# Kernel tuning notes

Measured on AMD Instinct MI355X. Metric: run time of the kernel, lower is better.

## Reference

```python
import jax, jax.numpy as jnp
import numpy as np

EPS = 1e-5

def _layernorm(x, gamma, beta):
    mu = jnp.mean(x, axis=-1, keepdims=True)
    var = jnp.var(x, axis=-1, keepdims=True)
    return (x - mu) * jax.lax.rsqrt(var + EPS) * gamma + beta

def setup_inputs() -> dict:
    key = jax.random.key(0)
    ks = jax.random.split(key, 6)
    bs, t, dim = 4, 2048, 1024
    x = jax.random.normal(ks[0], (bs, t, dim), dtype=jnp.float32)
    # shared LayerNorm params (same module applied twice in forward)
    ln_gamma = jnp.ones((dim,), dtype=jnp.float32)
    ln_beta = jnp.zeros((dim,), dtype=jnp.float32)
    # Linear params, stored as (in, out)
    w1 = jax.random.normal(ks[1], (dim, 2 * dim), dtype=jnp.float32) / np.sqrt(dim)
    b1 = jax.random.normal(ks[2], (2 * dim,), dtype=jnp.float32) * 0.01
    w2 = jax.random.normal(ks[3], (2 * dim, dim), dtype=jnp.float32) / np.sqrt(2 * dim)
    b2 = jax.random.normal(ks[4], (dim,), dtype=jnp.float32) * 0.01
    return {"x": x, "ln_gamma": ln_gamma, "ln_beta": ln_beta,
            "w1": w1, "b1": b1, "w2": w2, "b2": b2}

def reference(x, ln_gamma, ln_beta, w1, b1, w2, b2):
    # x: [bs, t, f]
    y = _layernorm(x, ln_gamma, ln_beta)
    y = jax.nn.gelu(jnp.einsum('btf,fh->bth', y, w1) + b1, approximate=False)
    y = jnp.einsum('bth,hf->btf', y, w2) + b2
    # attention-like quadratic mix (no softmax): (x @ x^T) @ y
    scores = jnp.einsum('btf,bsf->bts', x, x)          # [bs, t, t]
    y = jnp.einsum('bts,bsf->btf', scores, y)
    y = x + y
    y = _layernorm(y, ln_gamma, ln_beta)
    return y
```

## Files before the change

kernel.cpp:

```cpp
#include <hip/hip_runtime.h>
#include <hip/hip_fp16.h>

typedef _Float16 f16;
typedef _Float16 f16x8 __attribute__((ext_vector_type(8)));
typedef _Float16 f16x4 __attribute__((ext_vector_type(4)));
typedef float f32x4 __attribute__((ext_vector_type(4)));

#define LN_EPS 1e-5f

__device__ __forceinline__ float erf_fast(float x) {
    const float ax = __builtin_fabsf(x);
    const float t = 1.0f / (1.0f + 0.3275911f * ax);
    const float y = t * (0.254829592f +
                    t * (-0.284496736f +
                    t * (1.421413741f +
                    t * (-1.453152027f +
                    t * 1.061405429f))));
    const float r = 1.0f - y * __expf(-ax * ax);
    return __builtin_copysignf(r, x);
}

__device__ __forceinline__ float gelu_exact(float v) {
    return 0.5f * v * (1.0f + erf_fast(v * 0.70710678118654752440f));
}

__device__ __forceinline__ void gload_lds16(const f16* g, f16* l) {
    __builtin_amdgcn_global_load_lds(
        (const __attribute__((address_space(1))) unsigned int*)(g),
        (__attribute__((address_space(3))) unsigned int*)(l),
        16, 0, 0);
}

__global__ __launch_bounds__(256)
void ln_cast_kernel(const float* __restrict__ x,
                    const float* __restrict__ gamma,
                    const float* __restrict__ beta,
                    f16* __restrict__ y_h,
                    f16* __restrict__ x_h) {
    const int row = blockIdx.x;
    const int t = threadIdx.x;
    const size_t base = (size_t)row * 1024;
    float4 v = ((const float4*)(x + base))[t];
    float s  = v.x + v.y + v.z + v.w;
    float s2 = v.x*v.x + v.y*v.y + v.z*v.z + v.w*v.w;
    #pragma unroll
    for (int off = 32; off > 0; off >>= 1) {
        s  += __shfl_down(s, off, 64);
        s2 += __shfl_down(s2, off, 64);
    }
    __shared__ float ls[4], ls2[4];
    const int wid = t >> 6;
    if ((t & 63) == 0) { ls[wid] = s; ls2[wid] = s2; }
    __syncthreads();
    if (t == 0) {
        ls[0]  = ls[0] + ls[1] + ls[2] + ls[3];
        ls2[0] = ls2[0] + ls2[1] + ls2[2] + ls2[3];
    }
    __syncthreads();
    const float mu   = ls[0] * (1.0f / 1024.0f);
    const float var  = ls2[0] * (1.0f / 1024.0f) - mu * mu;
    const float rstd = rsqrtf(var + LN_EPS);
    const float4 g  = ((const float4*)gamma)[t];
    const float4 bt = ((const float4*)beta)[t];
    f16x4 yo, xo;
    yo[0] = (f16)((v.x - mu) * rstd * g.x + bt.x);
    yo[1] = (f16)((v.y - mu) * rstd * g.y + bt.y);
    yo[2] = (f16)((v.z - mu) * rstd * g.z + bt.z);
    yo[3] = (f16)((v.w - mu) * rstd * g.w + bt.w);
    xo[0] = (f16)v.x; xo[1] = (f16)v.y; xo[2] = (f16)v.z; xo[3] = (f16)v.w;
    *(f16x4*)(y_h + base + t * 4) = yo;
    *(f16x4*)(x_h + base + t * 4) = xo;
}

__global__ __launch_bounds__(256)
void ln_final_kernel(const float* __restrict__ pre,
                     const float* __restrict__ gamma,
                     const float* __restrict__ beta,
                     float* __restrict__ out) {
    const int row = blockIdx.x;
    const int t = threadIdx.x;
    const size_t base = (size_t)row * 1024;
    float4 v = ((const float4*)(pre + base))[t];
    float s  = v.x + v.y + v.z + v.w;
    float s2 = v.x*v.x + v.y*v.y + v.z*v.z + v.w*v.w;
    #pragma unroll
    for (int off = 32; off > 0; off >>= 1) {
        s  += __shfl_down(s, off, 64);
        s2 += __shfl_down(s2, off, 64);
    }
    __shared__ float ls[4], ls2[4];
    const int wid = t >> 6;
    if ((t & 63) == 0) { ls[wid] = s; ls2[wid] = s2; }
    __syncthreads();
    if (t == 0) {
        ls[0]  = ls[0] + ls[1] + ls[2] + ls[3];
        ls2[0] = ls2[0] + ls2[1] + ls2[2] + ls2[3];
    }
    __syncthreads();
    const float mu   = ls[0] * (1.0f / 1024.0f);
    const float var  = ls2[0] * (1.0f / 1024.0f) - mu * mu;
    const float rstd = rsqrtf(var + LN_EPS);
    const float4 g  = ((const float4*)gamma)[t];
    const float4 bt = ((const float4*)beta)[t];
    float4 o;
    o.x = (v.x - mu) * rstd * g.x + bt.x;
    o.y = (v.y - mu) * rstd * g.y + bt.y;
    o.z = (v.z - mu) * rstd * g.z + bt.z;
    o.w = (v.w - mu) * rstd * g.w + bt.w;
    ((float4*)(out + base))[t] = o;
}

__global__ __launch_bounds__(256)
void transpose_cast_kernel(const float* __restrict__ src,
                           f16* __restrict__ dst, int R, int C) {
    __shared__ float tile[32][33];
    const int c0 = blockIdx.x * 32, r0 = blockIdx.y * 32;
    const int tx = threadIdx.x & 31, ty = threadIdx.x >> 5;
    #pragma unroll
    for (int i = 0; i < 4; ++i) {
        const int r = ty + i * 8;
        tile[r][tx] = src[(size_t)(r0 + r) * C + c0 + tx];
    }
    __syncthreads();
    #pragma unroll
    for (int i = 0; i < 4; ++i) {
        const int r = ty + i * 8;
        dst[(size_t)(c0 + r) * R + r0 + tx] = (f16)tile[tx][r];
    }
}

__global__ __launch_bounds__(256)
void transpose_f16_kernel(const f16* __restrict__ src,
                          f16* __restrict__ dst, int R, int C) {
    __shared__ f16 tile[32][33];
    const size_t zb = (size_t)blockIdx.z * R * C;
    src += zb; dst += zb;
    const int c0 = blockIdx.x * 32, r0 = blockIdx.y * 32;
    const int tx = threadIdx.x & 31, ty = threadIdx.x >> 5;
    #pragma unroll
    for (int i = 0; i < 4; ++i) {
        const int r = ty + i * 8;
        tile[r][tx] = src[(size_t)(r0 + r) * C + c0 + tx];
    }
    __syncthreads();
    #pragma unroll
    for (int i = 0; i < 4; ++i) {
        const int r = ty + i * 8;
        dst[(size_t)(c0 + r) * R + r0 + tx] = tile[tx][r];
    }
}

template <int EPI>
__global__ __launch_bounds__(512, 2)
void gemm256x128_nt_kernel(const f16* __restrict__ A, const f16* __restrict__ Bt,
                           const float* __restrict__ bias,
                           const float* __restrict__ xadd,
                           f16* __restrict__ outH, float* __restrict__ outF,
                           int M, int N, int K,
                           long long batchA, long long batchB, long long batchC) {
    __shared__ __attribute__((aligned(16))) f16 sA[3][256 * 64];
    __shared__ __attribute__((aligned(16))) f16 sB[3][128 * 64];

    const int z = blockIdx.z;
    A  += (size_t)z * batchA;
    Bt += (size_t)z * batchB;

    const int m0 = blockIdx.x * 256;
    const int n0 = blockIdx.y * 128;
    const int t = threadIdx.x;
    const int l = t & 63;
    const int wid = t >> 6;
    const int wr = wid >> 1;
    const int wc = wid & 1;
    const int rl = l & 15;
    const int g  = l >> 4;
    const int nk = K >> 6;

    const int rowS = t >> 3;
    const int kbS  = ((t & 7) ^ (rowS & 7)) * 8;
    const f16* pA = A  + (size_t)(m0 + rowS) * K + kbS;
    const f16* pB = Bt + (size_t)(n0 + rowS) * K + kbS;
    const int ldsS = wid * 512;

    const int rA = wr * 64 + rl;
    const int rB = wc * 64 + rl;
    const int swk0 = ((g)     ^ (rl & 7)) * 8;
    const int swk1 = ((4 + g) ^ (rl & 7)) * 8;

    f32x4 acc[4][4] = {};

    auto mf = [&](f32x4 c, f16x8 af, f16x8 bf) {
        if constexpr (EPI != 1)
            return __builtin_amdgcn_mfma_f32_16x16x32_f16(bf, af, c, 0, 0, 0);
        else
            return __builtin_amdgcn_mfma_f32_16x16x32_f16(af, bf, c, 0, 0, 0);
    };

    auto stgA = [&](f16* dst, int u, int kc) {
        gload_lds16(pA + (size_t)u * 64 * K + kc * 64, dst + u * 4096 + ldsS);
    };
    auto stgB = [&](f16* dst, int u, int kc) {
        gload_lds16(pB + (size_t)u * 64 * K + kc * 64, dst + u * 4096 + ldsS);
    };

    const int t1 = (nk > 1) ? 1 : 0;
    #pragma unroll
    for (int u = 0; u < 4; ++u) stgA(sA[0], u, 0);
    #pragma unroll
    for (int u = 0; u < 2; ++u) stgB(sB[0], u, 0);
    #pragma unroll
    for (int u = 0; u < 4; ++u) stgA(sA[1], u, t1);
    #pragma unroll
    for (int u = 0; u < 2; ++u) stgB(sB[1], u, t1);

    f16 *curA = sA[0], *nxtA = sA[1], *farA = sA[2];
    f16 *curB = sB[0], *nxtB = sB[1], *farB = sB[2];

    f16x8 a[4][2], b[4][2];

    for (int kt = 0; kt < nk; ++kt) {
        asm volatile("s_waitcnt vmcnt(6)" ::: "memory");
        __builtin_amdgcn_s_barrier();

        const int kt2 = (kt + 2 < nk) ? kt + 2 : nk - 1;

        #pragma unroll
        for (int fm = 0; fm < 2; ++fm) {
            a[fm][0] = *(const f16x8*)(curA + (rA + fm * 16) * 64 + swk0);
            a[fm][1] = *(const f16x8*)(curA + (rA + fm * 16) * 64 + swk1);
        }
        #pragma unroll
        for (int fn = 0; fn < 2; ++fn) {
            b[fn][0] = *(const f16x8*)(curB + (rB + fn * 16) * 64 + swk0);
            b[fn][1] = *(const f16x8*)(curB + (rB + fn * 16) * 64 + swk1);
        }
        stgA(farA, 0, kt2);
        stgA(farA, 1, kt2);
        asm volatile("s_waitcnt lgkmcnt(0)" ::: "memory");
        __builtin_amdgcn_sched_barrier(0);
        __builtin_amdgcn_s_setprio(1);
        #pragma unroll
        for (int fm = 0; fm < 2; ++fm)
            #pragma unroll
            for (int fn = 0; fn < 2; ++fn) {
                acc[fm][fn] = mf(acc[fm][fn], a[fm][0], b[fn][0]);
                acc[fm][fn] = mf(acc[fm][fn], a[fm][1], b[fn][1]);
            }
        __builtin_amdgcn_s_setprio(0);

        #pragma unroll
        for (int fn = 2; fn < 4; ++fn) {
            b[fn][0] = *(const f16x8*)(curB + (rB + fn * 16) * 64 + swk0);
            b[fn][1] = *(const f16x8*)(curB + (rB + fn * 16) * 64 + swk1);
        }
        stgA(farA, 2, kt2);
        stgA(farA, 3, kt2);
        asm volatile("s_waitcnt lgkmcnt(0)" ::: "memory");
        __builtin_amdgcn_sched_barrier(0);
        __builtin_amdgcn_s_setprio(1);
        #pragma unroll
        for (int fm = 0; fm < 2; ++fm)
            #pragma unroll
            for (int fn = 2; fn < 4; ++fn) {
                acc[fm][fn] = mf(acc[fm][fn], a[fm][0], b[fn][0]);
                acc[fm][fn] = mf(acc[fm][fn], a[fm][1], b[fn][1]);
            }
        __builtin_amdgcn_s_setprio(0);

        #pragma unroll
        for (int fm = 2; fm < 4; ++fm) {
            a[fm][0] = *(const f16x8*)(curA + (rA + fm * 16) * 64 + swk0);
            a[fm][1] = *(const f16x8*)(curA + (rA + fm * 16) * 64 + swk1);
        }
        stgB(farB, 0, kt2);
        stgB(farB, 1, kt2);
        asm volatile("s_waitcnt lgkmcnt(0)" ::: "memory");
        __builtin_amdgcn_sched_barrier(0);
        __builtin_amdgcn_s_setprio(1);
        #pragma unroll
        for (int fm = 2; fm < 4; ++fm)
            #pragma unroll
            for (int fn = 2; fn < 4; ++fn) {
                acc[fm][fn] = mf(acc[fm][fn], a[fm][0], b[fn][0]);
                acc[fm][fn] = mf(acc[fm][fn], a[fm][1], b[fn][1]);
            }
        __builtin_amdgcn_s_setprio(0);

        __builtin_amdgcn_s_setprio(1);
        #pragma unroll
        for (int fm = 2; fm < 4; ++fm)
            #pragma unroll
            for (int fn = 0; fn < 2; ++fn) {
                acc[fm][fn] = mf(acc[fm][fn], a[fm][0], b[fn][0]);
                acc[fm][fn] = mf(acc[fm][fn], a[fm][1], b[fn][1]);
            }
        __builtin_amdgcn_s_setprio(0);

        f16* tp;
        tp = curA; curA = nxtA; nxtA = farA; farA = tp;
        tp = curB; curB = nxtB; nxtB = farB; farB = tp;
    }
    asm volatile("s_waitcnt vmcnt(0)" ::: "memory");

    if (EPI == 1) {
        #pragma unroll
        for (int fm = 0; fm < 4; ++fm) {
            #pragma unroll
            for (int fn = 0; fn < 4; ++fn) {
                const int col = n0 + wc * 64 + fn * 16 + rl;
                const int row0 = m0 + wr * 64 + fm * 16 + g * 4;
                const int zz = row0 >> 11;
                const int rr = row0 & 2047;
                const float bv = bias[col];
                f16x4 o;
                #pragma unroll
                for (int r = 0; r < 4; ++r) o[r] = (f16)(acc[fm][fn][r] + bv);
                *(f16x4*)(outH + ((size_t)zz * N + col) * 2048 + rr) = o;
            }
        }
    } else {
        const float* xaddz = xadd;
        float* outFz = outF;
        if (EPI == 3) {
            outFz += (size_t)z * batchC;
            xaddz += (size_t)z * batchC;
        }
        #pragma unroll
        for (int fm = 0; fm < 4; ++fm) {
            const int row = m0 + wr * 64 + fm * 16 + rl;
            #pragma unroll
            for (int fn = 0; fn < 4; ++fn) {
                const int colb = n0 + wc * 64 + fn * 16 + g * 4;
                if (EPI == 0) {
                    const float4 bv = *(const float4*)&bias[colb];
                    f16x4 o;
                    o[0] = (f16)gelu_exact(acc[fm][fn][0] + bv.x);
                    o[1] = (f16)gelu_exact(acc[fm][fn][1] + bv.y);
                    o[2] = (f16)gelu_exact(acc[fm][fn][2] + bv.z);
                    o[3] = (f16)gelu_exact(acc[fm][fn][3] + bv.w);
                    *(f16x4*)(outH + (size_t)row * N + colb) = o;
                } else {
                    const size_t idx = (size_t)row * N + colb;
                    const float4 xa = *(const float4*)&xaddz[idx];
                    float4 o;
                    o.x = acc[fm][fn][0] + xa.x;
                    o.y = acc[fm][fn][1] + xa.y;
                    o.z = acc[fm][fn][2] + xa.z;
                    o.w = acc[fm][fn][3] + xa.w;
                    *(float4*)(outFz + idx) = o;
                }
            }
        }
    }
}

__global__ __launch_bounds__(256, 3)
void gemm_nt_kernel(const f16* __restrict__ A, const f16* __restrict__ Bt,
                    f16* __restrict__ outH,
                    int M, int N, int K,
                    long long batchA, long long batchB, long long batchC) {
    __shared__ __attribute__((aligned(16))) f16 sA[3][128 * 32];
    __shared__ __attribute__((aligned(16))) f16 sB[3][128 * 32];

    const int z = blockIdx.z;
    A  += (size_t)z * batchA;
    Bt += (size_t)z * batchB;

    const int m0 = blockIdx.x * 128;
    const int n0 = blockIdx.y * 128;
    const int t = threadIdx.x;
    const int l = t & 63;
    const int wid = t >> 6;
    const int wm = (wid >> 1) * 64;
    const int wn = (wid & 1) * 64;

    f32x4 acc[4][4] = {};

    const int rl = l & 15;
    const int nk = K >> 5;

    const int row0 = t >> 2;
    const int kb = ((t & 3) ^ (row0 & 3)) * 8;
    const f16* Ag0 = A  + (size_t)(m0 + row0) * K + kb;
    const f16* Ag1 = A  + (size_t)(m0 + row0 + 64) * K + kb;
    const f16* Bg0 = Bt + (size_t)(n0 + row0) * K + kb;
    const f16* Bg1 = Bt + (size_t)(n0 + row0 + 64) * K + kb;
    const int lo0 = wid * 512;
    const int lo1 = 2048 + wid * 512;

    const int swk = (((l >> 4) ^ (rl & 3))) * 8;

    gload_lds16(Ag0,      sA[0] + lo0);
    gload_lds16(Ag1,      sA[0] + lo1);
    gload_lds16(Bg0,      sB[0] + lo0);
    gload_lds16(Bg1,      sB[0] + lo1);
    gload_lds16(Ag0 + 32, sA[1] + lo0);
    gload_lds16(Ag1 + 32, sA[1] + lo1);
    gload_lds16(Bg0 + 32, sB[1] + lo0);
    gload_lds16(Bg1 + 32, sB[1] + lo1);

    f16 *curA = sA[0], *nxtA = sA[1], *farA = sA[2];
    f16 *curB = sB[0], *nxtB = sB[1], *farB = sB[2];

    for (int kt = 0; kt < nk; ++kt) {
        asm volatile("s_waitcnt vmcnt(4)" ::: "memory");
        __builtin_amdgcn_s_barrier();

        const int ktn = (kt + 2 < nk) ? kt + 2 : nk - 1;
        const int kof = ktn * 32;
        gload_lds16(Ag0 + kof, farA + lo0);
        gload_lds16(Ag1 + kof, farA + lo1);
        gload_lds16(Bg0 + kof, farB + lo0);
        gload_lds16(Bg1 + kof, farB + lo1);

        f16x8 a[4], b[4];
        #pragma unroll
        for (int f = 0; f < 4; ++f) {
            a[f] = *(const f16x8*)&curA[(wm + f * 16 + rl) * 32 + swk];
            b[f] = *(const f16x8*)&curB[(wn + f * 16 + rl) * 32 + swk];
        }
        #pragma unroll
        for (int fm = 0; fm < 4; ++fm)
            #pragma unroll
            for (int fn = 0; fn < 4; ++fn)
                acc[fm][fn] = __builtin_amdgcn_mfma_f32_16x16x32_f16(
                    b[fn], a[fm], acc[fm][fn], 0, 0, 0);

        f16* tA = curA; curA = nxtA; nxtA = farA; farA = tA;
        f16* tB = curB; curB = nxtB; nxtB = farB; farB = tB;
    }
    asm volatile("s_waitcnt vmcnt(0)" ::: "memory");

    const int rh = l >> 4;
    f16* outHz = outH + (size_t)z * batchC;
    #pragma unroll
    for (int fm = 0; fm < 4; ++fm) {
        const int row = m0 + wm + fm * 16 + rl;
        #pragma unroll
        for (int fn = 0; fn < 4; ++fn) {
            const int colb = n0 + wn + fn * 16 + rh * 4;
            f16x4 o;
            #pragma unroll
            for (int r = 0; r < 4; ++r) o[r] = (f16)acc[fm][fn][r];
            *(f16x4*)(outHz + (size_t)row * N + colb) = o;
        }
    }
}

extern "C" void kernel_launch(void* const* d_in, const int* in_sizes, int n_in,
                              void* d_out, int out_size, void* d_ws, size_t ws_size,
                              hipStream_t stream) {
    const float* x     = (const float*)d_in[0];
    const float* gamma = (const float*)d_in[1];
    const float* beta  = (const float*)d_in[2];
    const float* w1    = (const float*)d_in[3];
    const float* b1    = (const float*)d_in[4];
    const float* w2    = (const float*)d_in[5];
    const float* b2    = (const float*)d_in[6];
    float* out = (float*)d_out;

    const int BS = 4, T = 2048, DIM = 1024, HID = 2048;
    const int M = BS * T;
    const long long MB = 1024 * 1024;

    char* ws = (char*)d_ws;
    f16*   x_h  = (f16*)(ws + 0 * MB);
    f16*   y_h  = (f16*)(ws + 16 * MB);
    f16*   h    = (f16*)(ws + 32 * MB);
    float* pre  = (float*)h;
    f16*   y2t  = (f16*)(ws + 64 * MB);
    f16*   x_t  = (f16*)(ws + 80 * MB);
    f16*   G    = (f16*)(ws + 96 * MB);
    f16*   w1t  = (f16*)(ws + 104 * MB);
    f16*   w2t  = (f16*)(ws + 108 * MB);

    ln_cast_kernel<<<M, 256, 0, stream>>>(x, gamma, beta, y_h, x_h);

    transpose_cast_kernel<<<dim3(HID / 32, DIM / 32), 256, 0, stream>>>(w1, w1t, DIM, HID);
    transpose_cast_kernel<<<dim3(DIM / 32, HID / 32), 256, 0, stream>>>(w2, w2t, HID, DIM);

    gemm256x128_nt_kernel<0><<<dim3(M / 256, HID / 128, 1), 512, 0, stream>>>(
        y_h, w1t, b1, nullptr, h, nullptr, M, HID, DIM, 0, 0, 0);

    gemm256x128_nt_kernel<1><<<dim3(M / 256, DIM / 128, 1), 512, 0, stream>>>(
        h, w2t, b2, nullptr, y2t, nullptr, M, DIM, HID, 0, 0, 0);

    transpose_f16_kernel<<<dim3(DIM / 32, T / 32, BS), 256, 0, stream>>>(x_h, x_t, T, DIM);

    gemm_nt_kernel<<<dim3(DIM / 128, DIM / 128, BS), 256, 0, stream>>>(
        y2t, x_t, G, DIM, DIM, T,
        (long long)DIM * T, (long long)DIM * T, (long long)DIM * DIM);

    gemm256x128_nt_kernel<3><<<dim3(T / 256, DIM / 128, BS), 512, 0, stream>>>(
        x_h, G, nullptr, x, nullptr, pre, T, DIM, DIM,
        (long long)T * DIM, (long long)DIM * DIM, (long long)T * DIM);

    ln_final_kernel<<<M, 256, 0, stream>>>(pre, gamma, beta, out);
}
```

Baseline: 202.1 us.

## Stage transposed GEMM2 epilogue through LDS and store pre-LN residual in fp16

```diff
diff --git a/kernel.cpp b/kernel.cpp
--- a/kernel.cpp
+++ b/kernel.cpp
@@ -73,14 +73,16 @@
 }
 
 __global__ __launch_bounds__(256)
-void ln_final_kernel(const float* __restrict__ pre,
+void ln_final_kernel(const f16* __restrict__ pre,
                      const float* __restrict__ gamma,
                      const float* __restrict__ beta,
                      float* __restrict__ out) {
     const int row = blockIdx.x;
     const int t = threadIdx.x;
     const size_t base = (size_t)row * 1024;
-    float4 v = ((const float4*)(pre + base))[t];
+    const f16x4 vh = *(const f16x4*)(pre + base + t * 4);
+    float4 v;
+    v.x = (float)vh[0]; v.y = (float)vh[1]; v.z = (float)vh[2]; v.w = (float)vh[3];
     float s  = v.x + v.y + v.z + v.w;
     float s2 = v.x*v.x + v.y*v.y + v.z*v.z + v.w*v.w;
     #pragma unroll
@@ -155,7 +157,7 @@
 void gemm256x128_nt_kernel(const f16* __restrict__ A, const f16* __restrict__ Bt,
                            const float* __restrict__ bias,
                            const float* __restrict__ xadd,
-                           f16* __restrict__ outH, float* __restrict__ outF,
+                           f16* __restrict__ outH,
                            int M, int N, int K,
                            long long batchA, long long batchB, long long batchC) {
     __shared__ __attribute__((aligned(16))) f16 sA[3][256 * 64];
@@ -300,29 +302,39 @@
         tp = curA; curA = nxtA; nxtA = farA; farA = tp;
         tp = curB; curB = nxtB; nxtB = farB; farB = tp;
     }
-    asm volatile("s_waitcnt vmcnt(0)" ::: "memory");
 
     if (EPI == 1) {
+        __syncthreads();
+        f16* lds_t = (f16*)sA;
         #pragma unroll
         for (int fm = 0; fm < 4; ++fm) {
+            const int rowb = wr * 64 + fm * 16 + g * 4;
             #pragma unroll
             for (int fn = 0; fn < 4; ++fn) {
-                const int col = n0 + wc * 64 + fn * 16 + rl;
-                const int row0 = m0 + wr * 64 + fm * 16 + g * 4;
-                const int zz = row0 >> 11;
-                const int rr = row0 & 2047;
-                const float bv = bias[col];
+                const int cl = wc * 64 + fn * 16 + rl;
+                const float bv = bias[n0 + cl];
                 f16x4 o;
                 #pragma unroll
                 for (int r = 0; r < 4; ++r) o[r] = (f16)(acc[fm][fn][r] + bv);
-                *(f16x4*)(outH + ((size_t)zz * N + col) * 2048 + rr) = o;
+                *(f16x4*)&lds_t[cl * 264 + rowb] = o;
             }
         }
+        __syncthreads();
+        const int lh = l & 31, ch = l >> 5;
+        #pragma unroll
+        for (int it = 0; it < 8; ++it) {
+            const int c = it * 16 + wid * 2 + ch;
+            const f16x8 vv = *(const f16x8*)&lds_t[c * 264 + lh * 8];
+            const int rowg = m0 + lh * 8;
+            const int zz = rowg >> 11, rr = rowg & 2047;
+            *(f16x8*)(outH + ((size_t)zz * N + (n0 + c)) * 2048 + rr) = vv;
+        }
     } else {
+        asm volatile("s_waitcnt vmcnt(0)" ::: "memory");
         const float* xaddz = xadd;
-        float* outFz = outF;
+        f16* outHz = outH;
         if (EPI == 3) {
-            outFz += (size_t)z * batchC;
+            outHz += (size_t)z * batchC;
             xaddz += (size_t)z * batchC;
         }
         #pragma unroll
@@ -342,12 +354,12 @@
                 } else {
                     const size_t idx = (size_t)row * N + colb;
                     const float4 xa = *(const float4*)&xaddz[idx];
-                    float4 o;
-                    o.x = acc[fm][fn][0] + xa.x;
-                    o.y = acc[fm][fn][1] + xa.y;
-                    o.z = acc[fm][fn][2] + xa.z;
-                    o.w = acc[fm][fn][3] + xa.w;
-                    *(float4*)(outFz + idx) = o;
+                    f16x4 o;
+                    o[0] = (f16)(acc[fm][fn][0] + xa.x);
+                    o[1] = (f16)(acc[fm][fn][1] + xa.y);
+                    o[2] = (f16)(acc[fm][fn][2] + xa.z);
+                    o[3] = (f16)(acc[fm][fn][3] + xa.w);
+                    *(f16x4*)(outHz + idx) = o;
                 }
             }
         }
@@ -405,6 +417,7 @@
     for (int kt = 0; kt < nk; ++kt) {
         asm volatile("s_waitcnt vmcnt(4)" ::: "memory");
         __builtin_amdgcn_s_barrier();
+        asm volatile("" ::: "memory");
 
         const int ktn = (kt + 2 < nk) ? kt + 2 : nk - 1;
         const int kof = ktn * 32;
@@ -464,15 +477,15 @@
     const long long MB = 1024 * 1024;
 
     char* ws = (char*)d_ws;
-    f16*   x_h  = (f16*)(ws + 0 * MB);
-    f16*   y_h  = (f16*)(ws + 16 * MB);
-    f16*   h    = (f16*)(ws + 32 * MB);
-    float* pre  = (float*)h;
-    f16*   y2t  = (f16*)(ws + 64 * MB);
-    f16*   x_t  = (f16*)(ws + 80 * MB);
-    f16*   G    = (f16*)(ws + 96 * MB);
-    f16*   w1t  = (f16*)(ws + 104 * MB);
-    f16*   w2t  = (f16*)(ws + 108 * MB);
+    f16*   x_h   = (f16*)(ws + 0 * MB);
+    f16*   y_h   = (f16*)(ws + 16 * MB);
+    f16*   h     = (f16*)(ws + 32 * MB);
+    f16*   pre_h = h;
+    f16*   y2t   = (f16*)(ws + 64 * MB);
+    f16*   x_t   = (f16*)(ws + 80 * MB);
+    f16*   G     = (f16*)(ws + 96 * MB);
+    f16*   w1t   = (f16*)(ws + 104 * MB);
+    f16*   w2t   = (f16*)(ws + 108 * MB);
 
     ln_cast_kernel<<<M, 256, 0, stream>>>(x, gamma, beta, y_h, x_h);
 
@@ -480,10 +493,10 @@
     transpose_cast_kernel<<<dim3(DIM / 32, HID / 32), 256, 0, stream>>>(w2, w2t, HID, DIM);
 
     gemm256x128_nt_kernel<0><<<dim3(M / 256, HID / 128, 1), 512, 0, stream>>>(
-        y_h, w1t, b1, nullptr, h, nullptr, M, HID, DIM, 0, 0, 0);
+        y_h, w1t, b1, nullptr, h, M, HID, DIM, 0, 0, 0);
 
     gemm256x128_nt_kernel<1><<<dim3(M / 256, DIM / 128, 1), 512, 0, stream>>>(
-        h, w2t, b2, nullptr, y2t, nullptr, M, DIM, HID, 0, 0, 0);
+        h, w2t, b2, nullptr, y2t, M, DIM, HID, 0, 0, 0);
 
     transpose_f16_kernel<<<dim3(DIM / 32, T / 32, BS), 256, 0, stream>>>(x_h, x_t, T, DIM);
 
@@ -492,8 +505,8 @@
         (long long)DIM * T, (long long)DIM * T, (long long)DIM * DIM);
 
     gemm256x128_nt_kernel<3><<<dim3(T / 256, DIM / 128, BS), 512, 0, stream>>>(
-        x_h, G, nullptr, x, nullptr, pre, T, DIM, DIM,
+        x_h, G, nullptr, x, pre_h, T, DIM, DIM,
         (long long)T * DIM, (long long)DIM * DIM, (long long)T * DIM);
 
-    ln_final_kernel<<<M, 256, 0, stream>>>(pre, gamma, beta, out);
-}
+    ln_final_kernel<<<M, 256, 0, stream>>>(pre_h, gamma, beta, out);
+}
```

Result: faster. 197.7 us (-2.2%).
